# Performance work log

Measured on AMD Instinct MI355X. Metric: run time of the kernel, lower is better.

## Reference

```python
import jax, jax.numpy as jnp
import numpy as np

B, H, N, D = 2, 16, 2048, 128

def setup_inputs() -> dict:
    key = jax.random.key(0)
    kq, kk, kv = jax.random.split(key, 3)
    q = jax.random.normal(kq, (B, H, N, D), dtype=jnp.float32)
    k = jax.random.normal(kk, (B, H, N, D), dtype=jnp.float32)
    v = jax.random.normal(kv, (B, H, N, D), dtype=jnp.float32)
    return {"q": q, "k": k, "v": v}

def reference(q, k, v):
    # scale = 1/sqrt(d) computed at forward time (scale=None in __init__)
    d = q.shape[-1]
    scale = 1.0 / jnp.sqrt(jnp.asarray(d, dtype=q.dtype))
    # scores: (B, H, N, N)
    scores = jnp.einsum('bhnd,bhmd->bhnm', q, k) * scale
    probs = jax.nn.softmax(scores, axis=-1)
    return jnp.einsum('bhnm,bhmd->bhnd', probs, v)
```

## Files before the change

### kernel.cpp

```cpp
#include <hip/hip_runtime.h>
#include <hip/hip_fp16.h>

#define BH   32
#define SEQ  2048
#define DIM  128
#define CK   32
#define NCH  (SEQ / CK)

typedef _Float16 half8   __attribute__((ext_vector_type(8)));
typedef __fp16   fp16x2  __attribute__((ext_vector_type(2)));
typedef _Float16 half2v  __attribute__((ext_vector_type(2)));
typedef float    floatx4 __attribute__((ext_vector_type(4)));

__device__ inline half2v pk2(float a, float b) {
    fp16x2 t = __builtin_amdgcn_cvt_pkrtz(a, b);
    return *(half2v*)&t;
}
__device__ inline half8 pk8(float4 a, float4 b) {
    half2v l0 = pk2(a.x, a.y), l1 = pk2(a.z, a.w);
    half2v l2 = pk2(b.x, b.y), l3 = pk2(b.z, b.w);
    half8 h;
    h[0] = l0[0]; h[1] = l0[1]; h[2] = l1[0]; h[3] = l1[1];
    h[4] = l2[0]; h[5] = l2[1]; h[6] = l3[0]; h[7] = l3[1];
    return h;
}

__device__ inline void ld16(const void* g, void* l) {
    __builtin_amdgcn_global_load_lds(
        (__attribute__((address_space(1))) void*)(uintptr_t)g,
        (__attribute__((address_space(3))) void*)(uintptr_t)l, 16, 0, 0);
}

#define SYNC_VM0 do {                                          \
    asm volatile("s_waitcnt vmcnt(0)" ::: "memory");           \
    __builtin_amdgcn_s_barrier();                              \
    asm volatile("" ::: "memory");                             \
} while (0)

__global__ void prep_kernel(const float* __restrict__ k, const float* __restrict__ v,
                            _Float16* __restrict__ kh, _Float16* __restrict__ vt) {
    const float SC = 0.08838834764831845f * 1.4426950408889634f;
    __shared__ __align__(16) _Float16 t[32][136];
    const int bh = blockIdx.x >> 6;
    const int kc = blockIdx.x & 63;
    const int tid = threadIdx.x;
    const size_t base = ((size_t)bh * SEQ + kc * CK) * DIM;

    const float4* kf4 = (const float4*)(k + base);
    const float4* vf4 = (const float4*)(v + base);
    half8* kh8 = (half8*)(kh + base);

    #pragma unroll
    for (int i = 0; i < 2; i++) {
        int f8 = i * 256 + tid;
        float4 a = kf4[2 * f8], b = kf4[2 * f8 + 1];
        a.x *= SC; a.y *= SC; a.z *= SC; a.w *= SC;
        b.x *= SC; b.y *= SC; b.z *= SC; b.w *= SC;
        kh8[f8] = pk8(a, b);
        int row = f8 >> 4, c8 = f8 & 15;
        *((half8*)&t[row][c8 * 8]) = pk8(vf4[2 * f8], vf4[2 * f8 + 1]);
    }
    __syncthreads();
    _Float16* vout = vt + ((size_t)bh * NCH + kc) * (DIM * CK);
    #pragma unroll
    for (int i = 0; i < 2; i++) {
        int g = i * 256 + tid;
        int d = g >> 2, kg = g & 3;
        half8 h;
        #pragma unroll
        for (int j = 0; j < 8; j++) h[j] = t[kg * 8 + j][d];
        *((half8*)(vout + d * CK + kg * 8)) = h;
    }
}

__global__ __launch_bounds__(256, 2) void attn_kernel(
        const float* __restrict__ q, const _Float16* __restrict__ kh,
        const _Float16* __restrict__ vt, float* __restrict__ out) {
    __shared__ __align__(16) _Float16 Kbuf[2][CK * DIM];
    __shared__ __align__(16) _Float16 Vbuf[3][DIM * CK];

    const int lid = blockIdx.x + (blockIdx.y << 4);
    const int xcd = lid & 7;
    const int idx = lid >> 3;
    const int bh  = (xcd << 2) + (idx >> 4);
    const int qt  = idx & 15;

    const int tid  = threadIdx.x;
    const int w    = tid >> 6;
    const int lane = tid & 63;
    const int l15  = lane & 15;
    const int quad = lane >> 4;

    half8 qf[2][4];
    #pragma unroll
    for (int s = 0; s < 2; s++) {
        const float* qb = q + ((size_t)bh * SEQ + qt * 128 + w * 32 + s * 16 + l15) * DIM;
        #pragma unroll
        for (int c = 0; c < 4; c++) {
            float4 a = *((const float4*)(qb + c * 32 + quad * 8));
            float4 b = *((const float4*)(qb + c * 32 + quad * 8 + 4));
            qf[s][c] = pk8(a, b);
        }
    }

    half8 ones;
    #pragma unroll
    for (int j = 0; j < 8; j++) ones[j] = (_Float16)1.0f;

    floatx4 zf = {0.f, 0.f, 0.f, 0.f};
    floatx4 O[2][8];
    #pragma unroll
    for (int s = 0; s < 2; s++)
        #pragma unroll
        for (int i = 0; i < 8; i++) O[s][i] = zf;
    floatx4 Osum[2] = {zf, zf};

    const _Float16* kb = kh + (size_t)bh * SEQ * DIM;
    const _Float16* vb = vt + (size_t)bh * SEQ * DIM;

    const int s0 = w * 128 + lane;
    const int s1 = s0 + 64;
    const int rho0 = s0 >> 4, Pos0 = s0 & 15;
    const int rho1 = s1 >> 4, Pos1 = s1 & 15;
    const int g0 = (Pos0 - 3 * rho0) & 15;
    const int g1 = (Pos1 - 3 * rho1) & 15;
    const int key0 = (((rho0 >> 2) & 3) << 3) + ((rho0 >> 4) << 2) + (rho0 & 3);
    const int key1 = (((rho1 >> 2) & 3) << 3) + ((rho1 >> 4) << 2) + (rho1 & 3);
    const _Float16* kgp0 = kb + key0 * DIM + g0 * 8;
    const _Float16* kgp1 = kb + key1 * DIM + g1 * 8;
    const int vo0 = ((s0 >> 6) * 16 + (s0 & 15)) * CK + ((s0 >> 4) & 3) * 8;
    const int vo1 = ((s1 >> 6) * 16 + (s1 & 15)) * CK + ((s1 >> 4) & 3) * 8;
    const _Float16* vgp0 = vb + vo0;
    const _Float16* vgp1 = vb + vo1;

    auto dma = [&](int kc, int bk_, int bv_) {
        size_t off = (size_t)kc * (CK * DIM);
        ld16(kgp0 + off, &Kbuf[bk_][(w * 2 + 0) * 512]);
        ld16(kgp1 + off, &Kbuf[bk_][(w * 2 + 1) * 512]);
        ld16(vgp0 + off, &Vbuf[bv_][(w * 2 + 0) * 512]);
        ld16(vgp1 + off, &Vbuf[bv_][(w * 2 + 1) * 512]);
    };

    half8 pf0, pf1;
    half8 vfr[8];
    #pragma unroll
    for (int j = 0; j < 8; j++) { pf0[j] = (_Float16)0.0f; pf1[j] = (_Float16)0.0f; }
    #pragma unroll
    for (int dt = 0; dt < 8; dt++)
        #pragma unroll
        for (int j = 0; j < 8; j++) vfr[dt][j] = (_Float16)0.0f;

    dma(0, 0, 0);

    int bvr = 0, bvn = 1;
    #pragma unroll 2
    for (int kc = 0; kc < NCH; kc++) {
        SYNC_VM0;
        if (kc + 1 < NCH) dma(kc + 1, (kc + 1) & 1, bvn);

        const _Float16* Kc = Kbuf[kc & 1];
        const _Float16* Vc = Vbuf[bvr];

        half8 ka[4];
        #pragma unroll
        for (int c = 0; c < 2; c++)
            #pragma unroll
            for (int j = 0; j < 2; j++) {
                int rho = j * 16 + l15;
                int Pos = (c * 4 + quad + 3 * rho) & 15;
                ka[c * 2 + j] = *((const half8*)&Kc[rho * DIM + Pos * 8]);
            }

        __builtin_amdgcn_s_setprio(1);
        Osum[0] = __builtin_amdgcn_mfma_f32_16x16x32_f16(pf0, ones, Osum[0], 0, 0, 0);
        #pragma unroll
        for (int dt = 0; dt < 8; dt++)
            O[0][dt] = __builtin_amdgcn_mfma_f32_16x16x32_f16(pf0, vfr[dt], O[0][dt], 0, 0, 0);
        __builtin_amdgcn_s_setprio(0);

        half8 kb2[4];
        #pragma unroll
        for (int c = 0; c < 2; c++)
            #pragma unroll
            for (int j = 0; j < 2; j++) {
                int rho = j * 16 + l15;
                int Pos = ((c + 2) * 4 + quad + 3 * rho) & 15;
                kb2[c * 2 + j] = *((const half8*)&Kc[rho * DIM + Pos * 8]);
            }

        __builtin_amdgcn_s_setprio(1);
        Osum[1] = __builtin_amdgcn_mfma_f32_16x16x32_f16(pf1, ones, Osum[1], 0, 0, 0);
        #pragma unroll
        for (int dt = 0; dt < 8; dt++)
            O[1][dt] = __builtin_amdgcn_mfma_f32_16x16x32_f16(pf1, vfr[dt], O[1][dt], 0, 0, 0);
        __builtin_amdgcn_s_setprio(0);

        floatx4 S[2][2];
        #pragma unroll
        for (int s = 0; s < 2; s++) { S[s][0] = zf; S[s][1] = zf; }
        __builtin_amdgcn_s_setprio(1);
        #pragma unroll
        for (int c = 0; c < 2; c++)
            #pragma unroll
            for (int j = 0; j < 2; j++) {
                S[0][j] = __builtin_amdgcn_mfma_f32_16x16x32_f16(ka[c * 2 + j], qf[0][c], S[0][j], 0, 0, 0);
                S[1][j] = __builtin_amdgcn_mfma_f32_16x16x32_f16(ka[c * 2 + j], qf[1][c], S[1][j], 0, 0, 0);
            }
        #pragma unroll
        for (int c = 0; c < 2; c++)
            #pragma unroll
            for (int j = 0; j < 2; j++) {
                S[0][j] = __builtin_amdgcn_mfma_f32_16x16x32_f16(kb2[c * 2 + j], qf[0][c + 2], S[0][j], 0, 0, 0);
                S[1][j] = __builtin_amdgcn_mfma_f32_16x16x32_f16(kb2[c * 2 + j], qf[1][c + 2], S[1][j], 0, 0, 0);
            }
        __builtin_amdgcn_s_setprio(0);

        #pragma unroll
        for (int dt = 0; dt < 8; dt++)
            vfr[dt] = *((const half8*)&Vc[dt * 512 + (quad * 16 + l15) * 8]);

        {
            float4 a, b;
            a.x = __builtin_amdgcn_exp2f(S[0][0][0]);
            a.y = __builtin_amdgcn_exp2f(S[0][0][1]);
            a.z = __builtin_amdgcn_exp2f(S[0][0][2]);
            a.w = __builtin_amdgcn_exp2f(S[0][0][3]);
            b.x = __builtin_amdgcn_exp2f(S[0][1][0]);
            b.y = __builtin_amdgcn_exp2f(S[0][1][1]);
            b.z = __builtin_amdgcn_exp2f(S[0][1][2]);
            b.w = __builtin_amdgcn_exp2f(S[0][1][3]);
            pf0 = pk8(a, b);
            a.x = __builtin_amdgcn_exp2f(S[1][0][0]);
            a.y = __builtin_amdgcn_exp2f(S[1][0][1]);
            a.z = __builtin_amdgcn_exp2f(S[1][0][2]);
            a.w = __builtin_amdgcn_exp2f(S[1][0][3]);
            b.x = __builtin_amdgcn_exp2f(S[1][1][0]);
            b.y = __builtin_amdgcn_exp2f(S[1][1][1]);
            b.z = __builtin_amdgcn_exp2f(S[1][1][2]);
            b.w = __builtin_amdgcn_exp2f(S[1][1][3]);
            pf1 = pk8(a, b);
        }

        bvr++; if (bvr == 3) bvr = 0;
        bvn++; if (bvn == 3) bvn = 0;
    }

    {
        __builtin_amdgcn_s_setprio(1);
        Osum[0] = __builtin_amdgcn_mfma_f32_16x16x32_f16(pf0, ones, Osum[0], 0, 0, 0);
        Osum[1] = __builtin_amdgcn_mfma_f32_16x16x32_f16(pf1, ones, Osum[1], 0, 0, 0);
        #pragma unroll
        for (int dt = 0; dt < 8; dt++) {
            O[0][dt] = __builtin_amdgcn_mfma_f32_16x16x32_f16(pf0, vfr[dt], O[0][dt], 0, 0, 0);
            O[1][dt] = __builtin_amdgcn_mfma_f32_16x16x32_f16(pf1, vfr[dt], O[1][dt], 0, 0, 0);
        }
        __builtin_amdgcn_s_setprio(0);
    }

    #pragma unroll
    for (int s = 0; s < 2; s++) {
        float* ob = out + ((size_t)bh * SEQ + qt * 128 + w * 32 + s * 16) * DIM;
        #pragma unroll
        for (int r = 0; r < 4; r++) {
            float rinv = 1.0f / Osum[s][r];
            #pragma unroll
            for (int dt = 0; dt < 8; dt++) {
                ob[(size_t)(quad * 4 + r) * DIM + dt * 16 + l15] = O[s][dt][r] * rinv;
            }
        }
    }
}

extern "C" void kernel_launch(void* const* d_in, const int* in_sizes, int n_in,
                              void* d_out, int out_size, void* d_ws, size_t ws_size,
                              hipStream_t stream) {
    const float* q = (const float*)d_in[0];
    const float* k = (const float*)d_in[1];
    const float* v = (const float*)d_in[2];
    float* out = (float*)d_out;

    const size_t elems = (size_t)BH * SEQ * DIM;
    _Float16* kh = (_Float16*)d_ws;
    _Float16* vtp = kh + elems;

    prep_kernel<<<BH * NCH, 256, 0, stream>>>(k, v, kh, vtp);
    attn_kernel<<<dim3(SEQ / 128, BH), 256, 0, stream>>>(q, kh, vtp, out);
}
```

Before: 194.5 us.

## Load two key chunks per barrier stage to halve synchronization count

Restructures the KV loop so each pipeline stage DMA-loads two 32-key chunks of K and V into double-buffered shared memory, then processes both chunks before the next barrier. This halves the number of vmcnt waits and block barriers across the sequence. The wait now also drains lgkmcnt, replacing the triple-buffered V ring. LDS use rises from 5 to 8 chunk-sized buffers, about 64KB, which may affect the two-blocks-per-CU occupancy target.

```diff
diff --git a/kernel.cpp b/kernel.cpp
--- a/kernel.cpp
+++ b/kernel.cpp
@@ -6,6 +6,8 @@
 #define DIM  128
 #define CK   32
 #define NCH  (SEQ / CK)
+#define NSUP (NCH / 2)
+#define CSZ  (CK * DIM)
 
 typedef _Float16 half8   __attribute__((ext_vector_type(8)));
 typedef __fp16   fp16x2  __attribute__((ext_vector_type(2)));
@@ -31,10 +33,10 @@
         (__attribute__((address_space(3))) void*)(uintptr_t)l, 16, 0, 0);
 }
 
-#define SYNC_VM0 do {                                          \
-    asm volatile("s_waitcnt vmcnt(0)" ::: "memory");           \
-    __builtin_amdgcn_s_barrier();                              \
-    asm volatile("" ::: "memory");                             \
+#define SYNC_VML do {                                              \
+    asm volatile("s_waitcnt vmcnt(0) lgkmcnt(0)" ::: "memory");    \
+    __builtin_amdgcn_s_barrier();                                  \
+    asm volatile("" ::: "memory");                                 \
 } while (0)
 
 __global__ void prep_kernel(const float* __restrict__ k, const float* __restrict__ v,
@@ -76,8 +78,8 @@
 __global__ __launch_bounds__(256, 2) void attn_kernel(
         const float* __restrict__ q, const _Float16* __restrict__ kh,
         const _Float16* __restrict__ vt, float* __restrict__ out) {
-    __shared__ __align__(16) _Float16 Kbuf[2][CK * DIM];
-    __shared__ __align__(16) _Float16 Vbuf[3][DIM * CK];
+    __shared__ __align__(16) _Float16 Kbuf[2][2 * CSZ];
+    __shared__ __align__(16) _Float16 Vbuf[2][2 * CSZ];
 
     const int lid = blockIdx.x + (blockIdx.y << 4);
     const int xcd = lid & 7;
@@ -133,12 +135,17 @@
     const _Float16* vgp0 = vb + vo0;
     const _Float16* vgp1 = vb + vo1;
 
-    auto dma = [&](int kc, int bk_, int bv_) {
-        size_t off = (size_t)kc * (CK * DIM);
-        ld16(kgp0 + off, &Kbuf[bk_][(w * 2 + 0) * 512]);
-        ld16(kgp1 + off, &Kbuf[bk_][(w * 2 + 1) * 512]);
-        ld16(vgp0 + off, &Vbuf[bv_][(w * 2 + 0) * 512]);
-        ld16(vgp1 + off, &Vbuf[bv_][(w * 2 + 1) * 512]);
+    auto dma2 = [&](int t, int b_) {
+        size_t off0 = (size_t)(2 * t) * CSZ;
+        size_t off1 = off0 + CSZ;
+        ld16(kgp0 + off0, &Kbuf[b_][(w * 2 + 0) * 512]);
+        ld16(kgp1 + off0, &Kbuf[b_][(w * 2 + 1) * 512]);
+        ld16(kgp0 + off1, &Kbuf[b_][CSZ + (w * 2 + 0) * 512]);
+        ld16(kgp1 + off1, &Kbuf[b_][CSZ + (w * 2 + 1) * 512]);
+        ld16(vgp0 + off0, &Vbuf[b_][(w * 2 + 0) * 512]);
+        ld16(vgp1 + off0, &Vbuf[b_][(w * 2 + 1) * 512]);
+        ld16(vgp0 + off1, &Vbuf[b_][CSZ + (w * 2 + 0) * 512]);
+        ld16(vgp1 + off1, &Vbuf[b_][CSZ + (w * 2 + 1) * 512]);
     };
 
     half8 pf0, pf1;
@@ -150,17 +157,7 @@
         #pragma unroll
         for (int j = 0; j < 8; j++) vfr[dt][j] = (_Float16)0.0f;
 
-    dma(0, 0, 0);
-
-    int bvr = 0, bvn = 1;
-    #pragma unroll 2
-    for (int kc = 0; kc < NCH; kc++) {
-        SYNC_VM0;
-        if (kc + 1 < NCH) dma(kc + 1, (kc + 1) & 1, bvn);
-
-        const _Float16* Kc = Kbuf[kc & 1];
-        const _Float16* Vc = Vbuf[bvr];
-
+    auto cbody = [&](const _Float16* Kc, const _Float16* Vc) {
         half8 ka[4];
         #pragma unroll
         for (int c = 0; c < 2; c++)
@@ -240,9 +237,18 @@
             b.w = __builtin_amdgcn_exp2f(S[1][1][3]);
             pf1 = pk8(a, b);
         }
-
-        bvr++; if (bvr == 3) bvr = 0;
-        bvn++; if (bvn == 3) bvn = 0;
+    };
+
+    dma2(0, 0);
+
+    #pragma unroll 2
+    for (int t = 0; t < NSUP; t++) {
+        SYNC_VML;
+        if (t + 1 < NSUP) dma2(t + 1, (t + 1) & 1);
+        const _Float16* Kc = Kbuf[t & 1];
+        const _Float16* Vc = Vbuf[t & 1];
+        cbody(Kc, Vc);
+        cbody(Kc + CSZ, Vc + CSZ);
     }
 
     {
```

Measured after the change: 192.9 us. Within noise of the previous version (-0.8%).

## Use 2 waves per block with 64 query rows per wave

Applied to the files above, without the earlier changes.

Cuts the attention block from 4 waves to 2, and each wave now handles 64 query rows (4 sub-tiles) instead of 32. Every K/V fragment read from LDS is reused across twice as many MFMAs, and each wave issues four async loads per tensor per chunk. The cost is roughly double the accumulator and register use per wave and half as many waves per block to hide latency. Launch bounds fall to (128,1), which may reduce occupancy.

```diff
diff --git a/kernel.cpp b/kernel.cpp
--- a/kernel.cpp
+++ b/kernel.cpp
@@ -6,6 +6,7 @@
 #define DIM  128
 #define CK   32
 #define NCH  (SEQ / CK)
+#define CSZ  (CK * DIM)
 
 typedef _Float16 half8   __attribute__((ext_vector_type(8)));
 typedef __fp16   fp16x2  __attribute__((ext_vector_type(2)));
@@ -73,11 +74,11 @@
     }
 }
 
-__global__ __launch_bounds__(256, 2) void attn_kernel(
+__global__ __launch_bounds__(128, 1) void attn_kernel(
         const float* __restrict__ q, const _Float16* __restrict__ kh,
         const _Float16* __restrict__ vt, float* __restrict__ out) {
-    __shared__ __align__(16) _Float16 Kbuf[2][CK * DIM];
-    __shared__ __align__(16) _Float16 Vbuf[3][DIM * CK];
+    __shared__ __align__(16) _Float16 Kbuf[2][CSZ];
+    __shared__ __align__(16) _Float16 Vbuf[3][CSZ];
 
     const int lid = blockIdx.x + (blockIdx.y << 4);
     const int xcd = lid & 7;
@@ -91,10 +92,10 @@
     const int l15  = lane & 15;
     const int quad = lane >> 4;
 
-    half8 qf[2][4];
-    #pragma unroll
-    for (int s = 0; s < 2; s++) {
-        const float* qb = q + ((size_t)bh * SEQ + qt * 128 + w * 32 + s * 16 + l15) * DIM;
+    half8 qf[4][4];
+    #pragma unroll
+    for (int s = 0; s < 4; s++) {
+        const float* qb = q + ((size_t)bh * SEQ + qt * 128 + w * 64 + s * 16 + l15) * DIM;
         #pragma unroll
         for (int c = 0; c < 4; c++) {
             float4 a = *((const float4*)(qb + c * 32 + quad * 8));
@@ -108,47 +109,131 @@
     for (int j = 0; j < 8; j++) ones[j] = (_Float16)1.0f;
 
     floatx4 zf = {0.f, 0.f, 0.f, 0.f};
-    floatx4 O[2][8];
-    #pragma unroll
-    for (int s = 0; s < 2; s++)
+    floatx4 O[4][8];
+    #pragma unroll
+    for (int s = 0; s < 4; s++)
         #pragma unroll
         for (int i = 0; i < 8; i++) O[s][i] = zf;
-    floatx4 Osum[2] = {zf, zf};
+    floatx4 Osum[4] = {zf, zf, zf, zf};
 
     const _Float16* kb = kh + (size_t)bh * SEQ * DIM;
     const _Float16* vb = vt + (size_t)bh * SEQ * DIM;
 
-    const int s0 = w * 128 + lane;
-    const int s1 = s0 + 64;
-    const int rho0 = s0 >> 4, Pos0 = s0 & 15;
-    const int rho1 = s1 >> 4, Pos1 = s1 & 15;
-    const int g0 = (Pos0 - 3 * rho0) & 15;
-    const int g1 = (Pos1 - 3 * rho1) & 15;
-    const int key0 = (((rho0 >> 2) & 3) << 3) + ((rho0 >> 4) << 2) + (rho0 & 3);
-    const int key1 = (((rho1 >> 2) & 3) << 3) + ((rho1 >> 4) << 2) + (rho1 & 3);
-    const _Float16* kgp0 = kb + key0 * DIM + g0 * 8;
-    const _Float16* kgp1 = kb + key1 * DIM + g1 * 8;
-    const int vo0 = ((s0 >> 6) * 16 + (s0 & 15)) * CK + ((s0 >> 4) & 3) * 8;
-    const int vo1 = ((s1 >> 6) * 16 + (s1 & 15)) * CK + ((s1 >> 4) & 3) * 8;
-    const _Float16* vgp0 = vb + vo0;
-    const _Float16* vgp1 = vb + vo1;
+    const _Float16* kgp[4];
+    const _Float16* vgp[4];
+    #pragma unroll
+    for (int i = 0; i < 4; i++) {
+        int si = w * 256 + i * 64 + lane;
+        int rho = si >> 4, Pos = si & 15;
+        int g = (Pos - 3 * rho) & 15;
+        int key = (((rho >> 2) & 3) << 3) + ((rho >> 4) << 2) + (rho & 3);
+        kgp[i] = kb + key * DIM + g * 8;
+        int vo = ((si >> 6) * 16 + (si & 15)) * CK + ((si >> 4) & 3) * 8;
+        vgp[i] = vb + vo;
+    }
 
     auto dma = [&](int kc, int bk_, int bv_) {
-        size_t off = (size_t)kc * (CK * DIM);
-        ld16(kgp0 + off, &Kbuf[bk_][(w * 2 + 0) * 512]);
-        ld16(kgp1 + off, &Kbuf[bk_][(w * 2 + 1) * 512]);
-        ld16(vgp0 + off, &Vbuf[bv_][(w * 2 + 0) * 512]);
-        ld16(vgp1 + off, &Vbuf[bv_][(w * 2 + 1) * 512]);
+        size_t off = (size_t)kc * CSZ;
+        #pragma unroll
+        for (int i = 0; i < 4; i++) {
+            ld16(kgp[i] + off, &Kbuf[bk_][w * 2048 + i * 512]);
+            ld16(vgp[i] + off, &Vbuf[bv_][w * 2048 + i * 512]);
+        }
     };
 
-    half8 pf0, pf1;
+    half8 pf[4];
     half8 vfr[8];
     #pragma unroll
-    for (int j = 0; j < 8; j++) { pf0[j] = (_Float16)0.0f; pf1[j] = (_Float16)0.0f; }
+    for (int s = 0; s < 4; s++)
+        #pragma unroll
+        for (int j = 0; j < 8; j++) pf[s][j] = (_Float16)0.0f;
     #pragma unroll
     for (int dt = 0; dt < 8; dt++)
         #pragma unroll
         for (int j = 0; j < 8; j++) vfr[dt][j] = (_Float16)0.0f;
+
+    auto body = [&](int bk_, int bvr_) {
+        const _Float16* Kc = Kbuf[bk_];
+        const _Float16* Vc = Vbuf[bvr_];
+
+        half8 ka[4];
+        #pragma unroll
+        for (int c = 0; c < 2; c++)
+            #pragma unroll
+            for (int j = 0; j < 2; j++) {
+                int rho = j * 16 + l15;
+                int Pos = (c * 4 + quad + 3 * rho) & 15;
+                ka[c * 2 + j] = *((const half8*)&Kc[rho * DIM + Pos * 8]);
+            }
+
+        __builtin_amdgcn_s_setprio(1);
+        #pragma unroll
+        for (int s = 0; s < 2; s++) {
+            Osum[s] = __builtin_amdgcn_mfma_f32_16x16x32_f16(pf[s], ones, Osum[s], 0, 0, 0);
+            #pragma unroll
+            for (int dt = 0; dt < 8; dt++)
+                O[s][dt] = __builtin_amdgcn_mfma_f32_16x16x32_f16(pf[s], vfr[dt], O[s][dt], 0, 0, 0);
+        }
+        __builtin_amdgcn_s_setprio(0);
+
+        half8 kb2[4];
+        #pragma unroll
+        for (int c = 0; c < 2; c++)
+            #pragma unroll
+            for (int j = 0; j < 2; j++) {
+                int rho = j * 16 + l15;
+                int Pos = ((c + 2) * 4 + quad + 3 * rho) & 15;
+                kb2[c * 2 + j] = *((const half8*)&Kc[rho * DIM + Pos * 8]);
+            }
+
+        __builtin_amdgcn_s_setprio(1);
+        #pragma unroll
+        for (int s = 2; s < 4; s++) {
+            Osum[s] = __builtin_amdgcn_mfma_f32_16x16x32_f16(pf[s], ones, Osum[s], 0, 0, 0);
+            #pragma unroll
+            for (int dt = 0; dt < 8; dt++)
+                O[s][dt] = __builtin_amdgcn_mfma_f32_16x16x32_f16(pf[s], vfr[dt], O[s][dt], 0, 0, 0);
+        }
+        __builtin_amdgcn_s_setprio(0);
+
+        floatx4 S[4][2];
+        #pragma unroll
+        for (int s = 0; s < 4; s++) { S[s][0] = zf; S[s][1] = zf; }
+        __builtin_amdgcn_s_setprio(1);
+        #pragma unroll
+        for (int c = 0; c < 2; c++)
+            #pragma unroll
+            for (int j = 0; j < 2; j++)
+                #pragma unroll
+                for (int s = 0; s < 4; s++)
+                    S[s][j] = __builtin_amdgcn_mfma_f32_16x16x32_f16(ka[c * 2 + j], qf[s][c], S[s][j], 0, 0, 0);
+        #pragma unroll
+        for (int c = 0; c < 2; c++)
+            #pragma unroll
+            for (int j = 0; j < 2; j++)
+                #pragma unroll
+                for (int s = 0; s < 4; s++)
+                    S[s][j] = __builtin_amdgcn_mfma_f32_16x16x32_f16(kb2[c * 2 + j], qf[s][c + 2], S[s][j], 0, 0, 0);
+        __builtin_amdgcn_s_setprio(0);
+
+        #pragma unroll
+        for (int dt = 0; dt < 8; dt++)
+            vfr[dt] = *((const half8*)&Vc[dt * 512 + (quad * 16 + l15) * 8]);
+
+        #pragma unroll
+        for (int s = 0; s < 4; s++) {
+            float4 a, b;
+            a.x = __builtin_amdgcn_exp2f(S[s][0][0]);
+            a.y = __builtin_amdgcn_exp2f(S[s][0][1]);
+            a.z = __builtin_amdgcn_exp2f(S[s][0][2]);
+            a.w = __builtin_amdgcn_exp2f(S[s][0][3]);
+            b.x = __builtin_amdgcn_exp2f(S[s][1][0]);
+            b.y = __builtin_amdgcn_exp2f(S[s][1][1]);
+            b.z = __builtin_amdgcn_exp2f(S[s][1][2]);
+            b.w = __builtin_amdgcn_exp2f(S[s][1][3]);
+            pf[s] = pk8(a, b);
+        }
+    };
 
     dma(0, 0, 0);
 
@@ -157,109 +242,24 @@
     for (int kc = 0; kc < NCH; kc++) {
         SYNC_VM0;
         if (kc + 1 < NCH) dma(kc + 1, (kc + 1) & 1, bvn);
-
-        const _Float16* Kc = Kbuf[kc & 1];
-        const _Float16* Vc = Vbuf[bvr];
-
-        half8 ka[4];
-        #pragma unroll
-        for (int c = 0; c < 2; c++)
-            #pragma unroll
-            for (int j = 0; j < 2; j++) {
-                int rho = j * 16 + l15;
-                int Pos = (c * 4 + quad + 3 * rho) & 15;
-                ka[c * 2 + j] = *((const half8*)&Kc[rho * DIM + Pos * 8]);
-            }
-
-        __builtin_amdgcn_s_setprio(1);
-        Osum[0] = __builtin_amdgcn_mfma_f32_16x16x32_f16(pf0, ones, Osum[0], 0, 0, 0);
-        #pragma unroll
-        for (int dt = 0; dt < 8; dt++)
-            O[0][dt] = __builtin_amdgcn_mfma_f32_16x16x32_f16(pf0, vfr[dt], O[0][dt], 0, 0, 0);
-        __builtin_amdgcn_s_setprio(0);
-
-        half8 kb2[4];
-        #pragma unroll
-        for (int c = 0; c < 2; c++)
-            #pragma unroll
-            for (int j = 0; j < 2; j++) {
-                int rho = j * 16 + l15;
-                int Pos = ((c + 2) * 4 + quad + 3 * rho) & 15;
-                kb2[c * 2 + j] = *((const half8*)&Kc[rho * DIM + Pos * 8]);
-            }
-
-        __builtin_amdgcn_s_setprio(1);
-        Osum[1] = __builtin_amdgcn_mfma_f32_16x16x32_f16(pf1, ones, Osum[1], 0, 0, 0);
-        #pragma unroll
-        for (int dt = 0; dt < 8; dt++)
-            O[1][dt] = __builtin_amdgcn_mfma_f32_16x16x32_f16(pf1, vfr[dt], O[1][dt], 0, 0, 0);
-        __builtin_amdgcn_s_setprio(0);
-
-        floatx4 S[2][2];
-        #pragma unroll
-        for (int s = 0; s < 2; s++) { S[s][0] = zf; S[s][1] = zf; }
-        __builtin_amdgcn_s_setprio(1);
-        #pragma unroll
-        for (int c = 0; c < 2; c++)
-            #pragma unroll
-            for (int j = 0; j < 2; j++) {
-                S[0][j] = __builtin_amdgcn_mfma_f32_16x16x32_f16(ka[c * 2 + j], qf[0][c], S[0][j], 0, 0, 0);
-                S[1][j] = __builtin_amdgcn_mfma_f32_16x16x32_f16(ka[c * 2 + j], qf[1][c], S[1][j], 0, 0, 0);
-            }
-        #pragma unroll
-        for (int c = 0; c < 2; c++)
-            #pragma unroll
-            for (int j = 0; j < 2; j++) {
-                S[0][j] = __builtin_amdgcn_mfma_f32_16x16x32_f16(kb2[c * 2 + j], qf[0][c + 2], S[0][j], 0, 0, 0);
-                S[1][j] = __builtin_amdgcn_mfma_f32_16x16x32_f16(kb2[c * 2 + j], qf[1][c + 2], S[1][j], 0, 0, 0);
-            }
-        __builtin_amdgcn_s_setprio(0);
-
-        #pragma unroll
-        for (int dt = 0; dt < 8; dt++)
-            vfr[dt] = *((const half8*)&Vc[dt * 512 + (quad * 16 + l15) * 8]);
-
-        {
-            float4 a, b;
-            a.x = __builtin_amdgcn_exp2f(S[0][0][0]);
-            a.y = __builtin_amdgcn_exp2f(S[0][0][1]);
-            a.z = __builtin_amdgcn_exp2f(S[0][0][2]);
-            a.w = __builtin_amdgcn_exp2f(S[0][0][3]);
-            b.x = __builtin_amdgcn_exp2f(S[0][1][0]);
-            b.y = __builtin_amdgcn_exp2f(S[0][1][1]);
-            b.z = __builtin_amdgcn_exp2f(S[0][1][2]);
-            b.w = __builtin_amdgcn_exp2f(S[0][1][3]);
-            pf0 = pk8(a, b);
-            a.x = __builtin_amdgcn_exp2f(S[1][0][0]);
-            a.y = __builtin_amdgcn_exp2f(S[1][0][1]);
-            a.z = __builtin_amdgcn_exp2f(S[1][0][2]);
-            a.w = __builtin_amdgcn_exp2f(S[1][0][3]);
-            b.x = __builtin_amdgcn_exp2f(S[1][1][0]);
-            b.y = __builtin_amdgcn_exp2f(S[1][1][1]);
-            b.z = __builtin_amdgcn_exp2f(S[1][1][2]);
-            b.w = __builtin_amdgcn_exp2f(S[1][1][3]);
-            pf1 = pk8(a, b);
-        }
-
+        body(kc & 1, bvr);
         bvr++; if (bvr == 3) bvr = 0;
         bvn++; if (bvn == 3) bvn = 0;
     }
 
-    {
-        __builtin_amdgcn_s_setprio(1);
-        Osum[0] = __builtin_amdgcn_mfma_f32_16x16x32_f16(pf0, ones, Osum[0], 0, 0, 0);
-        Osum[1] = __builtin_amdgcn_mfma_f32_16x16x32_f16(pf1, ones, Osum[1], 0, 0, 0);
-        #pragma unroll
-        for (int dt = 0; dt < 8; dt++) {
-            O[0][dt] = __builtin_amdgcn_mfma_f32_16x16x32_f16(pf0, vfr[dt], O[0][dt], 0, 0, 0);
-            O[1][dt] = __builtin_amdgcn_mfma_f32_16x16x32_f16(pf1, vfr[dt], O[1][dt], 0, 0, 0);
-        }
-        __builtin_amdgcn_s_setprio(0);
-    }
-
-    #pragma unroll
-    for (int s = 0; s < 2; s++) {
-        float* ob = out + ((size_t)bh * SEQ + qt * 128 + w * 32 + s * 16) * DIM;
+    __builtin_amdgcn_s_setprio(1);
+    #pragma unroll
+    for (int s = 0; s < 4; s++) {
+        Osum[s] = __builtin_amdgcn_mfma_f32_16x16x32_f16(pf[s], ones, Osum[s], 0, 0, 0);
+        #pragma unroll
+        for (int dt = 0; dt < 8; dt++)
+            O[s][dt] = __builtin_amdgcn_mfma_f32_16x16x32_f16(pf[s], vfr[dt], O[s][dt], 0, 0, 0);
+    }
+    __builtin_amdgcn_s_setprio(0);
+
+    #pragma unroll
+    for (int s = 0; s < 4; s++) {
+        float* ob = out + ((size_t)bh * SEQ + qt * 128 + w * 64 + s * 16) * DIM;
         #pragma unroll
         for (int r = 0; r < 4; r++) {
             float rinv = 1.0f / Osum[s][r];
@@ -284,5 +284,5 @@
     _Float16* vtp = kh + elems;
 
     prep_kernel<<<BH * NCH, 256, 0, stream>>>(k, v, kh, vtp);
-    attn_kernel<<<dim3(SEQ / 128, BH), 256, 0, stream>>>(q, kh, vtp, out);
-}
+    attn_kernel<<<dim3(SEQ / 128, BH), 128, 0, stream>>>(q, kh, vtp, out);
+}
```

After: 208.1 us. 7.0% more time.
